# Performance work log

Measured on AMD Instinct MI355X. Metric: run time of the kernel, lower is better.

Reference implementation:

```python
import jax, jax.numpy as jnp
import numpy as np

B, Nv, Ne, Dv, De, Du = 8, 4096, 32768, 128, 128, 128
Dep, Dvp, Dup = 128, 128, 128


def setup_inputs() -> dict:
    key = jax.random.key(0)
    ks = jax.random.split(key, 11)
    s = 0.02
    return {
        "nodes": jax.random.normal(ks[0], (B, Nv, Dv), jnp.float32),
        "edges": jax.random.normal(ks[1], (B, Ne, De), jnp.float32),
        "global_u": jax.random.normal(ks[2], (B, Du), jnp.float32),
        "edge_rs": jax.random.randint(ks[3], (B, Ne, 2), 0, Nv, jnp.int32),
        "edge_masks": jax.random.randint(ks[4], (B, Ne, 1), 0, 2, jnp.int32),
        "W_edge": jax.random.normal(ks[5], (De + 2 * Dv + Du, Dep), jnp.float32) * s,
        "b_edge": jnp.zeros((Dep,), jnp.float32),
        "W_node": jax.random.normal(ks[6], (Dep + Dv + Du, Dvp), jnp.float32) * s,
        "b_node": jnp.zeros((Dvp,), jnp.float32),
        "W_glob": jax.random.normal(ks[7], (Dep + Dvp + Du, Dup), jnp.float32) * s,
        "b_glob": jnp.zeros((Dup,), jnp.float32),
    }


def reference(nodes, edges, global_u, edge_rs, edge_masks,
              W_edge, b_edge, W_node, b_node, W_glob, b_glob):
    recv = edge_rs[..., 0]  # (B,Ne)
    send = edge_rs[..., 1]
    # gather receiver / sender node features: (B,Ne,Dv)
    r_nodes = jnp.take_along_axis(nodes, jnp.broadcast_to(recv[..., None], (B, Ne, Dv)), axis=1)
    s_nodes = jnp.take_along_axis(nodes, jnp.broadcast_to(send[..., None], (B, Ne, Dv)), axis=1)
    u_e = jnp.broadcast_to(global_u[:, None, :], (B, Ne, Du))

    # edge block: MLP on concat -> (B,Ne,Dep)
    edge_in = jnp.concatenate([edges, r_nodes, s_nodes, u_e], -1)
    edges_p = jax.nn.relu(edge_in @ W_edge + b_edge)

    # e2v merge: masked segment-sum of edges onto receiver nodes -> (B,Nv,Dep)
    mask = edge_masks.astype(edges_p.dtype)  # (B,Ne,1)
    e2v = jax.vmap(lambda e, r: jax.ops.segment_sum(e, r, num_segments=Nv))(edges_p * mask, recv)

    # node block
    u_n = jnp.broadcast_to(global_u[:, None, :], (B, Nv, Du))
    node_in = jnp.concatenate([e2v, nodes, u_n], -1)
    nodes_p = jax.nn.relu(node_in @ W_node + b_node)

    # global block: sum-pool edges and nodes
    e2u = edges_p.sum(axis=1)  # (B,Dep)
    v2u = nodes_p.sum(axis=1)  # (B,Dvp)
    global_in = jnp.concatenate([e2u, v2u, global_u], -1)
    global_u_p = jax.nn.relu(global_in @ W_glob + b_glob)

    return (nodes_p, edges_p, global_u_p)
```

## Files before the change

### kernel.cpp

```cpp
#include <hip/hip_runtime.h>
#include <hip/hip_bf16.h>

#define B  8
#define NV 4096
#define NE 32768
#define D  128
#define KE2 384
#define KN2 256
#define KG 384

using short8 = __attribute__((ext_vector_type(8))) short;
using f32x4  = __attribute__((ext_vector_type(4))) float;

__device__ inline unsigned short f2bf(float f) {
    unsigned u = __builtin_bit_cast(unsigned, f);
    u += 0x7FFFu + ((u >> 16) & 1u);
    return (unsigned short)(u >> 16);
}

__device__ inline short8 cvt8(float4 a, float4 b) {
    union { __hip_bfloat162 h[4]; short8 v; } u;
    u.h[0] = __float22bfloat162_rn(make_float2(a.x, a.y));
    u.h[1] = __float22bfloat162_rn(make_float2(a.z, a.w));
    u.h[2] = __float22bfloat162_rn(make_float2(b.x, b.y));
    u.h[3] = __float22bfloat162_rn(make_float2(b.z, b.w));
    return u.v;
}

__global__ __launch_bounds__(256) void prep_weights(
    const float* __restrict__ We, const float* __restrict__ Wn,
    unsigned short* __restrict__ WtE, unsigned short* __restrict__ WtN)
{
    const int idx = blockIdx.x * 256 + threadIdx.x;
    {
        const int n = idx / KE2, k = idx % KE2;
        WtE[idx] = f2bf(We[(size_t)k * D + n]);
    }
    if (idx < 128 * KN2) {
        const int n = idx >> 8, k = idx & 255;
        WtN[idx] = f2bf(Wn[(size_t)k * D + n]);
    }
}

__global__ __launch_bounds__(128) void bias_kernel(
    const float* __restrict__ gu,
    const float* __restrict__ We, const float* __restrict__ be,
    const float* __restrict__ Wn, const float* __restrict__ bn,
    float* __restrict__ bias_e, float* __restrict__ bias_n)
{
    const int b = blockIdx.x, n = threadIdx.x;
    float se = be[n], sn = bn[n];
    for (int k = 0; k < D; ++k) {
        const float uk = gu[(size_t)b * D + k];
        se += uk * We[(size_t)(KE2 + k) * D + n];
        sn += uk * Wn[(size_t)(KN2 + k) * D + n];
    }
    bias_e[(size_t)b * D + n] = se;
    bias_n[(size_t)b * D + n] = sn;
}

__global__ __launch_bounds__(256) void hist_kernel(
    const int* __restrict__ edge_rs, const int* __restrict__ edge_masks,
    int* __restrict__ cnt)
{
    const int idx = blockIdx.x * 256 + threadIdx.x;
    if (edge_masks[idx]) {
        const int b = idx >> 15;
        const int r = edge_rs[2 * idx];
        atomicAdd(cnt + b * NV + r, 1);
    }
}

__global__ __launch_bounds__(1024) void scan_kernel(
    const int* __restrict__ cnt, int* __restrict__ off, int* __restrict__ cur)
{
    const int b = blockIdx.x, t = threadIdx.x;
    __shared__ int part[1024];
    int4 c = *(const int4*)(cnt + b * NV + t * 4);
    const int s0 = c.x, s1 = s0 + c.y, s2 = s1 + c.z, s3 = s2 + c.w;
    part[t] = s3;
    __syncthreads();
    #pragma unroll
    for (int d = 1; d < 1024; d <<= 1) {
        const int v = (t >= d) ? part[t - d] : 0;
        __syncthreads();
        part[t] += v;
        __syncthreads();
    }
    const int base = part[t] - s3;
    int* o = off + b * (NV + 1) + t * 4;
    o[0] = base; o[1] = base + s0; o[2] = base + s1; o[3] = base + s2;
    int4 cc = { base, base + s0, base + s1, base + s2 };
    *(int4*)(cur + b * NV + t * 4) = cc;
    if (t == 1023) off[b * (NV + 1) + NV] = part[1023];
}

__global__ __launch_bounds__(256) void scatter_kernel(
    const int* __restrict__ edge_rs, const int* __restrict__ edge_masks,
    int* __restrict__ cur, int* __restrict__ elist)
{
    const int idx = blockIdx.x * 256 + threadIdx.x;
    if (edge_masks[idx]) {
        const int b = idx >> 15;
        const int e = idx & (NE - 1);
        const int r = edge_rs[2 * idx];
        const int pos = atomicAdd(cur + b * NV + r, 1);
        elist[b * NE + pos] = e;
    }
}

__global__ __launch_bounds__(512, 4) void edge_kernel(
    const float* __restrict__ nodes,
    const float* __restrict__ edges,
    const int*   __restrict__ edge_rs,
    const unsigned short* __restrict__ WtE,
    const float* __restrict__ bias_e,
    float* __restrict__ edges_p,
    float* __restrict__ pe)
{
    __shared__ unsigned short Albuf[2][128 * 64];
    __shared__ unsigned short Wlbuf[2][128 * 64];

    const int tid  = threadIdx.x;
    const int bid  = blockIdx.x;
    const int b    = bid & 7;
    const int tile = bid >> 3;
    const int e0   = tile * 128;

    const int srow = tid >> 2;
    const int sq   = tid & 3;
    const int sX   = (srow & 7) << 3;

    const int2 rs = ((const int2*)edge_rs)[(size_t)b * NE + e0 + srow];
    const float* aseg0 = edges + ((size_t)b * NE + e0 + srow) * D;
    const float* aseg1 = nodes + ((size_t)b * NV + rs.x) * D;
    const float* aseg2 = nodes + ((size_t)b * NV + rs.y) * D;

    const int lane = tid & 63;
    const int wv   = tid >> 6;
    const int wr   = wv >> 2, wc = wv & 3;
    const int lc   = lane & 15, lg = lane >> 4;
    const int lX   = (lc & 7) << 3;

    float4 av[2], av2[2];
    short8 wstg[2];

    auto loadA = [&](int t) {
        const float* seg = (t < 2) ? aseg0 : (t < 4) ? aseg1 : aseg2;
        const float* src = seg + (t & 1) * 64 + sq * 16;
        av[0]  = *(const float4*)(src);
        av[1]  = *(const float4*)(src + 4);
        av2[0] = *(const float4*)(src + 8);
        av2[1] = *(const float4*)(src + 12);
    };
    auto loadW = [&](int t) {
        const unsigned short* src = WtE + (size_t)srow * KE2 + t * 64 + sq * 16;
        wstg[0] = *(const short8*)(src);
        wstg[1] = *(const short8*)(src + 8);
    };
    auto writeStage = [&](int buf) {
        unsigned short* Al = Albuf[buf];
        unsigned short* Wl = Wlbuf[buf];
        const int g0 = sq * 16;
        *(short8*)(Al + srow * 64 + ((g0    ) ^ sX)) = cvt8(av[0], av[1]);
        *(short8*)(Al + srow * 64 + ((g0 + 8) ^ sX)) = cvt8(av2[0], av2[1]);
        *(short8*)(Wl + srow * 64 + ((g0    ) ^ sX)) = wstg[0];
        *(short8*)(Wl + srow * 64 + ((g0 + 8) ^ sX)) = wstg[1];
    };

    f32x4 acc[4][2] = {};
    auto compute = [&](int buf) {
        const unsigned short* Al = Albuf[buf];
        const unsigned short* Wl = Wlbuf[buf];
        #pragma unroll
        for (int ksub = 0; ksub < 2; ++ksub) {
            const int k = ksub * 32 + lg * 8;
            short8 afr[4], bfr[2];
            #pragma unroll
            for (int mt = 0; mt < 4; ++mt)
                afr[mt] = *(const short8*)(Al + (wr * 64 + mt * 16 + lc) * 64 + (k ^ lX));
            #pragma unroll
            for (int nt = 0; nt < 2; ++nt)
                bfr[nt] = *(const short8*)(Wl + (wc * 32 + nt * 16 + lc) * 64 + (k ^ lX));
            #pragma unroll
            for (int mt = 0; mt < 4; ++mt)
                #pragma unroll
                for (int nt = 0; nt < 2; ++nt)
                    acc[mt][nt] = __builtin_amdgcn_mfma_f32_16x16x32_bf16(
                                      afr[mt], bfr[nt], acc[mt][nt], 0, 0, 0);
        }
    };

    loadA(0); loadW(0); writeStage(0);
    __syncthreads();
    #pragma unroll
    for (int t = 0; t < 6; ++t) {
        if (t < 5) { loadA(t + 1); loadW(t + 1); }
        compute(t & 1);
        if (t < 5) writeStage((t + 1) & 1);
        __syncthreads();
    }

    #pragma unroll
    for (int nt = 0; nt < 2; ++nt) {
        const int col = wc * 32 + nt * 16 + lc;
        const float bias = bias_e[(size_t)b * D + col];
        float csum = 0.f;
        #pragma unroll
        for (int mt = 0; mt < 4; ++mt)
            #pragma unroll
            for (int r = 0; r < 4; ++r) {
                const int row = wr * 64 + mt * 16 + lg * 4 + r;
                const float v = fmaxf(acc[mt][nt][r] + bias, 0.f);
                edges_p[((size_t)b * NE + e0 + row) * D + col] = v;
                csum += v;
            }
        csum += __shfl_xor(csum, 16);
        csum += __shfl_xor(csum, 32);
        if (lg == 0)
            pe[(((size_t)b * 256 + tile) * 2 + wr) * D + col] = csum;
    }
}

__global__ __launch_bounds__(512, 4) void node_kernel(
    const float* __restrict__ nodes,
    const float* __restrict__ edges_p,
    const int*   __restrict__ off,
    const int*   __restrict__ elist,
    const unsigned short* __restrict__ WtN,
    const float* __restrict__ bias_n,
    float* __restrict__ nodes_p,
    float* __restrict__ pn)
{
    __shared__ unsigned short Albuf[2][128 * 64];
    __shared__ unsigned short Wlbuf[2][128 * 64];

    const int tid  = threadIdx.x;
    const int bid  = blockIdx.x;
    const int b    = bid & 7;
    const int tile = bid >> 3;
    const int n0   = tile * 128;

    const int srow = tid >> 2;
    const int sq   = tid & 3;
    const int sX   = (srow & 7) << 3;

    const int vtx = n0 + srow;
    const int p0  = off[b * (NV + 1) + vtx];
    const int p1  = off[b * (NV + 1) + vtx + 1];
    const float* nsrc = nodes + ((size_t)b * NV + vtx) * D;

    const int lane = tid & 63;
    const int wv   = tid >> 6;
    const int wr   = wv >> 2, wc = wv & 3;
    const int lc   = lane & 15, lg = lane >> 4;
    const int lX   = (lc & 7) << 3;

    float4 av[2], av2[2];
    short8 wstg[2];

    auto loadA = [&](int t) {
        if (t < 2) {
            float4 s0 = {}, s1 = {}, s2 = {}, s3 = {};
            const int koff = (t & 1) * 64 + sq * 16;
            for (int p = p0; p < p1; ++p) {
                const int e = elist[b * NE + p];
                const float* src = edges_p + ((size_t)b * NE + e) * D + koff;
                const float4 x0 = *(const float4*)(src);
                const float4 x1 = *(const float4*)(src + 4);
                const float4 x2 = *(const float4*)(src + 8);
                const float4 x3 = *(const float4*)(src + 12);
                s0.x += x0.x; s0.y += x0.y; s0.z += x0.z; s0.w += x0.w;
                s1.x += x1.x; s1.y += x1.y; s1.z += x1.z; s1.w += x1.w;
                s2.x += x2.x; s2.y += x2.y; s2.z += x2.z; s2.w += x2.w;
                s3.x += x3.x; s3.y += x3.y; s3.z += x3.z; s3.w += x3.w;
            }
            av[0] = s0; av[1] = s1; av2[0] = s2; av2[1] = s3;
        } else {
            const float* src = nsrc + (t - 2) * 64 + sq * 16;
            av[0]  = *(const float4*)(src);
            av[1]  = *(const float4*)(src + 4);
            av2[0] = *(const float4*)(src + 8);
            av2[1] = *(const float4*)(src + 12);
        }
    };
    auto loadW = [&](int t) {
        const unsigned short* src = WtN + (size_t)srow * KN2 + t * 64 + sq * 16;
        wstg[0] = *(const short8*)(src);
        wstg[1] = *(const short8*)(src + 8);
    };
    auto writeStage = [&](int buf) {
        unsigned short* Al = Albuf[buf];
        unsigned short* Wl = Wlbuf[buf];
        const int g0 = sq * 16;
        *(short8*)(Al + srow * 64 + ((g0    ) ^ sX)) = cvt8(av[0], av[1]);
        *(short8*)(Al + srow * 64 + ((g0 + 8) ^ sX)) = cvt8(av2[0], av2[1]);
        *(short8*)(Wl + srow * 64 + ((g0    ) ^ sX)) = wstg[0];
        *(short8*)(Wl + srow * 64 + ((g0 + 8) ^ sX)) = wstg[1];
    };

    f32x4 acc[4][2] = {};
    auto compute = [&](int buf) {
        const unsigned short* Al = Albuf[buf];
        const unsigned short* Wl = Wlbuf[buf];
        #pragma unroll
        for (int ksub = 0; ksub < 2; ++ksub) {
            const int k = ksub * 32 + lg * 8;
            short8 afr[4], bfr[2];
            #pragma unroll
            for (int mt = 0; mt < 4; ++mt)
                afr[mt] = *(const short8*)(Al + (wr * 64 + mt * 16 + lc) * 64 + (k ^ lX));
            #pragma unroll
            for (int nt = 0; nt < 2; ++nt)
                bfr[nt] = *(const short8*)(Wl + (wc * 32 + nt * 16 + lc) * 64 + (k ^ lX));
            #pragma unroll
            for (int mt = 0; mt < 4; ++mt)
                #pragma unroll
                for (int nt = 0; nt < 2; ++nt)
                    acc[mt][nt] = __builtin_amdgcn_mfma_f32_16x16x32_bf16(
                                      afr[mt], bfr[nt], acc[mt][nt], 0, 0, 0);
        }
    };

    loadA(0); loadW(0); writeStage(0);
    __syncthreads();
    #pragma unroll
    for (int t = 0; t < 4; ++t) {
        if (t < 3) { loadA(t + 1); loadW(t + 1); }
        compute(t & 1);
        if (t < 3) writeStage((t + 1) & 1);
        __syncthreads();
    }

    #pragma unroll
    for (int nt = 0; nt < 2; ++nt) {
        const int col = wc * 32 + nt * 16 + lc;
        const float bias = bias_n[(size_t)b * D + col];
        float csum = 0.f;
        #pragma unroll
        for (int mt = 0; mt < 4; ++mt)
            #pragma unroll
            for (int r = 0; r < 4; ++r) {
                const int row = wr * 64 + mt * 16 + lg * 4 + r;
                const float v = fmaxf(acc[mt][nt][r] + bias, 0.f);
                nodes_p[((size_t)b * NV + n0 + row) * D + col] = v;
                csum += v;
            }
        csum += __shfl_xor(csum, 16);
        csum += __shfl_xor(csum, 32);
        if (lg == 0)
            pn[(((size_t)b * 32 + tile) * 2 + wr) * D + col] = csum;
    }
}

__global__ __launch_bounds__(128) void reduce_kernel(
    const float* __restrict__ pe, const float* __restrict__ pn,
    float* __restrict__ e2u, float* __restrict__ v2u)
{
    const int b = blockIdx.x, j = threadIdx.x;
    float s = 0.f;
    for (int i = 0; i < 512; ++i) s += pe[((size_t)b * 512 + i) * D + j];
    e2u[(size_t)b * D + j] = s;
    float t = 0.f;
    for (int i = 0; i < 64; ++i) t += pn[((size_t)b * 64 + i) * D + j];
    v2u[(size_t)b * D + j] = t;
}

__global__ __launch_bounds__(128) void glob_kernel(
    const float* __restrict__ e2u,
    const float* __restrict__ v2u,
    const float* __restrict__ gu,
    const float* __restrict__ W_glob,
    const float* __restrict__ b_glob,
    float* __restrict__ glob_p)
{
    __shared__ float gin[KG];
    const int b = blockIdx.x;
    const int j = threadIdx.x;

    gin[j      ] = e2u[(size_t)b * D + j];
    gin[j + 128] = v2u[(size_t)b * D + j];
    gin[j + 256] = gu [(size_t)b * D + j];
    __syncthreads();

    float acc = b_glob[j];
    #pragma unroll 4
    for (int k = 0; k < KG; ++k)
        acc += gin[k] * W_glob[(size_t)k * D + j];
    glob_p[(size_t)b * D + j] = fmaxf(acc, 0.f);
}

extern "C" void kernel_launch(void* const* d_in, const int* in_sizes, int n_in,
                              void* d_out, int out_size, void* d_ws, size_t ws_size,
                              hipStream_t stream) {
    const float* nodes      = (const float*)d_in[0];
    const float* edges      = (const float*)d_in[1];
    const float* gu         = (const float*)d_in[2];
    const int*   edge_rs    = (const int*)d_in[3];
    const int*   edge_masks = (const int*)d_in[4];
    const float* W_edge     = (const float*)d_in[5];
    const float* b_edge     = (const float*)d_in[6];
    const float* W_node     = (const float*)d_in[7];
    const float* b_node     = (const float*)d_in[8];
    const float* W_glob     = (const float*)d_in[9];
    const float* b_glob     = (const float*)d_in[10];

    float* out     = (float*)d_out;
    float* nodes_p = out;
    float* edges_p = out + (size_t)B * NV * D;
    float* glob_p  = edges_p + (size_t)B * NE * D;

    int*   cnt    = (int*)d_ws;
    int*   off    = cnt + (size_t)B * NV;
    int*   cur    = off + (size_t)B * (NV + 1);
    int*   elist  = cur + (size_t)B * NV;
    float* e2u    = (float*)(elist + (size_t)B * NE);
    float* v2u    = e2u + (size_t)B * D;
    float* bias_e = v2u + (size_t)B * D;
    float* bias_n = bias_e + (size_t)B * D;
    float* pe     = bias_n + (size_t)B * D;
    float* pn     = pe + (size_t)B * 512 * D;
    unsigned short* WtE = (unsigned short*)(pn + (size_t)B * 64 * D);
    unsigned short* WtN = WtE + 128 * KE2;

    hipMemsetAsync(cnt, 0, (size_t)B * NV * sizeof(int), stream);

    prep_weights<<<(128 * KE2) / 256, 256, 0, stream>>>(W_edge, W_node, WtE, WtN);
    bias_kernel<<<B, 128, 0, stream>>>(gu, W_edge, b_edge, W_node, b_node, bias_e, bias_n);
    hist_kernel<<<(B * NE) / 256, 256, 0, stream>>>(edge_rs, edge_masks, cnt);
    scan_kernel<<<B, 1024, 0, stream>>>(cnt, off, cur);
    scatter_kernel<<<(B * NE) / 256, 256, 0, stream>>>(edge_rs, edge_masks, cur, elist);

    edge_kernel<<<(NE / 128) * B, 512, 0, stream>>>(nodes, edges, edge_rs,
                                                    WtE, bias_e, edges_p, pe);
    node_kernel<<<(NV / 128) * B, 512, 0, stream>>>(nodes, edges_p, off, elist,
                                                    WtN, bias_n, nodes_p, pn);
    reduce_kernel<<<B, 128, 0, stream>>>(pe, pn, e2u, v2u);
    glob_kernel<<<B, 128, 0, stream>>>(e2u, v2u, gu, W_glob, b_glob, glob_p);
}
```

Measured before the change: 190.6 us.

## Keep full edge weight in LDS and give each wave its own edge rows

The edge kernel now loads the whole bf16 edge weight matrix into shared memory once per block. Each wave then processes 16 edges against all 128 output columns, staging its activations in a private double buffer, so the block-wide barriers inside the K loop are gone. Outputs are written as float4 and partial column sums are produced per wave, which grows the partial-sum buffer; the reduce kernel is widened to 256 threads to sum the larger buffer. The cost is much larger shared-memory use per block, which cuts resident blocks per CU and may limit latency hiding for the gather-heavy loads, plus a full weight reload from L2 into every block.

Result: slower. 226.1 us (+18.6%).

```diff
diff --git a/kernel.cpp b/kernel.cpp
--- a/kernel.cpp
+++ b/kernel.cpp
@@ -9,8 +9,9 @@
 #define KN2 256
 #define KG 384
 
-using short8 = __attribute__((ext_vector_type(8))) short;
-using f32x4  = __attribute__((ext_vector_type(4))) float;
+using short8    = __attribute__((ext_vector_type(8))) short;
+using f32x4     = __attribute__((ext_vector_type(4))) float;
+using ushort4_t = __attribute__((ext_vector_type(4))) unsigned short;
 
 __device__ inline unsigned short f2bf(float f) {
     unsigned u = __builtin_bit_cast(unsigned, f);
@@ -118,8 +119,8 @@
     float* __restrict__ edges_p,
     float* __restrict__ pe)
 {
-    __shared__ unsigned short Albuf[2][128 * 64];
-    __shared__ unsigned short Wlbuf[2][128 * 64];
+    __shared__ unsigned short Wsh[6 * 128 * 64];
+    __shared__ unsigned short Abuf[8 * 2 * 16 * 64];
 
     const int tid  = threadIdx.x;
     const int bid  = blockIdx.x;
@@ -127,98 +128,97 @@
     const int tile = bid >> 3;
     const int e0   = tile * 128;
 
-    const int srow = tid >> 2;
-    const int sq   = tid & 3;
-    const int sX   = (srow & 7) << 3;
-
-    const int2 rs = ((const int2*)edge_rs)[(size_t)b * NE + e0 + srow];
-    const float* aseg0 = edges + ((size_t)b * NE + e0 + srow) * D;
-    const float* aseg1 = nodes + ((size_t)b * NV + rs.x) * D;
-    const float* aseg2 = nodes + ((size_t)b * NV + rs.y) * D;
+    {
+        const int c  = tid >> 2;
+        const int q  = tid & 3;
+        const int sX = (c & 7) << 3;
+        #pragma unroll
+        for (int t = 0; t < 6; ++t) {
+            const unsigned short* src = WtE + (size_t)c * KE2 + t * 64 + q * 16;
+            unsigned short* dst = Wsh + t * 128 * 64 + c * 64;
+            *(short8*)(dst + ((q * 16    ) ^ sX)) = *(const short8*)(src);
+            *(short8*)(dst + ((q * 16 + 8) ^ sX)) = *(const short8*)(src + 8);
+        }
+    }
+    __syncthreads();
 
     const int lane = tid & 63;
     const int wv   = tid >> 6;
-    const int wr   = wv >> 2, wc = wv & 3;
-    const int lc   = lane & 15, lg = lane >> 4;
-    const int lX   = (lc & 7) << 3;
-
-    float4 av[2], av2[2];
-    short8 wstg[2];
-
+    const int lc   = lane & 15;
+    const int lg   = lane >> 4;
+    const int sXl  = (lc & 7) << 3;
+
+    const int    ew = e0 + wv * 16;
+    const size_t eb = (size_t)b * NE + ew + lc;
+    const int2   rs = ((const int2*)edge_rs)[eb];
+    const float* pE = edges + eb * D;
+    const float* pR = nodes + ((size_t)b * NV + rs.x) * D;
+    const float* pS = nodes + ((size_t)b * NV + rs.y) * D;
+
+    unsigned short* Aw = Abuf + wv * 2048;
+
+    float4 av[4];
     auto loadA = [&](int t) {
-        const float* seg = (t < 2) ? aseg0 : (t < 4) ? aseg1 : aseg2;
-        const float* src = seg + (t & 1) * 64 + sq * 16;
-        av[0]  = *(const float4*)(src);
-        av[1]  = *(const float4*)(src + 4);
-        av2[0] = *(const float4*)(src + 8);
-        av2[1] = *(const float4*)(src + 12);
-    };
-    auto loadW = [&](int t) {
-        const unsigned short* src = WtE + (size_t)srow * KE2 + t * 64 + sq * 16;
-        wstg[0] = *(const short8*)(src);
-        wstg[1] = *(const short8*)(src + 8);
-    };
-    auto writeStage = [&](int buf) {
-        unsigned short* Al = Albuf[buf];
-        unsigned short* Wl = Wlbuf[buf];
-        const int g0 = sq * 16;
-        *(short8*)(Al + srow * 64 + ((g0    ) ^ sX)) = cvt8(av[0], av[1]);
-        *(short8*)(Al + srow * 64 + ((g0 + 8) ^ sX)) = cvt8(av2[0], av2[1]);
-        *(short8*)(Wl + srow * 64 + ((g0    ) ^ sX)) = wstg[0];
-        *(short8*)(Wl + srow * 64 + ((g0 + 8) ^ sX)) = wstg[1];
-    };
-
-    f32x4 acc[4][2] = {};
-    auto compute = [&](int buf) {
-        const unsigned short* Al = Albuf[buf];
-        const unsigned short* Wl = Wlbuf[buf];
+        const float* seg = (t < 2) ? pE : (t < 4) ? pR : pS;
+        const float* src = seg + (t & 1) * 64 + lg * 16;
+        av[0] = *(const float4*)(src);
+        av[1] = *(const float4*)(src + 4);
+        av[2] = *(const float4*)(src + 8);
+        av[3] = *(const float4*)(src + 12);
+    };
+    auto writeA = [&](int buf) {
+        unsigned short* dst = Aw + buf * 1024 + lc * 64;
+        *(short8*)(dst + ((lg * 16    ) ^ sXl)) = cvt8(av[0], av[1]);
+        *(short8*)(dst + ((lg * 16 + 8) ^ sXl)) = cvt8(av[2], av[3]);
+    };
+
+    f32x4 acc[8] = {};
+    auto compute = [&](int t, int buf) {
+        const unsigned short* Asrc = Aw + buf * 1024;
+        const unsigned short* Wt   = Wsh + t * 128 * 64;
         #pragma unroll
         for (int ksub = 0; ksub < 2; ++ksub) {
             const int k = ksub * 32 + lg * 8;
-            short8 afr[4], bfr[2];
+            const short8 afr = *(const short8*)(Asrc + lc * 64 + (k ^ sXl));
             #pragma unroll
-            for (int mt = 0; mt < 4; ++mt)
-                afr[mt] = *(const short8*)(Al + (wr * 64 + mt * 16 + lc) * 64 + (k ^ lX));
-            #pragma unroll
-            for (int nt = 0; nt < 2; ++nt)
-                bfr[nt] = *(const short8*)(Wl + (wc * 32 + nt * 16 + lc) * 64 + (k ^ lX));
-            #pragma unroll
-            for (int mt = 0; mt < 4; ++mt)
-                #pragma unroll
-                for (int nt = 0; nt < 2; ++nt)
-                    acc[mt][nt] = __builtin_amdgcn_mfma_f32_16x16x32_bf16(
-                                      afr[mt], bfr[nt], acc[mt][nt], 0, 0, 0);
+            for (int nt = 0; nt < 8; ++nt) {
+                const int col = nt * 16 + lc;
+                const short8 bfr = *(const short8*)(Wt + col * 64 + (k ^ ((col & 7) << 3)));
+                acc[nt] = __builtin_amdgcn_mfma_f32_16x16x32_bf16(bfr, afr, acc[nt], 0, 0, 0);
+            }
         }
     };
 
-    loadA(0); loadW(0); writeStage(0);
-    __syncthreads();
+    loadA(0);
+    writeA(0);
     #pragma unroll
     for (int t = 0; t < 6; ++t) {
-        if (t < 5) { loadA(t + 1); loadW(t + 1); }
-        compute(t & 1);
-        if (t < 5) writeStage((t + 1) & 1);
-        __syncthreads();
+        if (t < 5) loadA(t + 1);
+        compute(t, t & 1);
+        if (t < 5) writeA((t + 1) & 1);
     }
 
     #pragma unroll
-    for (int nt = 0; nt < 2; ++nt) {
-        const int col = wc * 32 + nt * 16 + lc;
-        const float bias = bias_e[(size_t)b * D + col];
-        float csum = 0.f;
+    for (int nt = 0; nt < 8; ++nt) {
+        const int f0 = nt * 16 + lg * 4;
+        const float4 bb = *(const float4*)(bias_e + (size_t)b * D + f0);
+        float4 o;
+        o.x = fmaxf(acc[nt][0] + bb.x, 0.f);
+        o.y = fmaxf(acc[nt][1] + bb.y, 0.f);
+        o.z = fmaxf(acc[nt][2] + bb.z, 0.f);
+        o.w = fmaxf(acc[nt][3] + bb.w, 0.f);
+        *(float4*)(edges_p + eb * D + f0) = o;
+
+        float4 ps = o;
         #pragma unroll
-        for (int mt = 0; mt < 4; ++mt)
-            #pragma unroll
-            for (int r = 0; r < 4; ++r) {
-                const int row = wr * 64 + mt * 16 + lg * 4 + r;
-                const float v = fmaxf(acc[mt][nt][r] + bias, 0.f);
-                edges_p[((size_t)b * NE + e0 + row) * D + col] = v;
-                csum += v;
-            }
-        csum += __shfl_xor(csum, 16);
-        csum += __shfl_xor(csum, 32);
-        if (lg == 0)
-            pe[(((size_t)b * 256 + tile) * 2 + wr) * D + col] = csum;
+        for (int m = 1; m < 16; m <<= 1) {
+            ps.x += __shfl_xor(ps.x, m);
+            ps.y += __shfl_xor(ps.y, m);
+            ps.z += __shfl_xor(ps.z, m);
+            ps.w += __shfl_xor(ps.w, m);
+        }
+        if (lc == 0)
+            *(float4*)(pe + (((size_t)b * 256 + tile) * 8 + wv) * D + f0) = ps;
     }
 }
 
@@ -353,17 +353,27 @@
     }
 }
 
-__global__ __launch_bounds__(128) void reduce_kernel(
+__global__ __launch_bounds__(256) void reduce_kernel(
     const float* __restrict__ pe, const float* __restrict__ pn,
     float* __restrict__ e2u, float* __restrict__ v2u)
 {
-    const int b = blockIdx.x, j = threadIdx.x;
+    __shared__ float redE[2][128], redN[2][128];
+    const int b = blockIdx.x;
+    const int j = threadIdx.x & 127;
+    const int h = threadIdx.x >> 7;
     float s = 0.f;
-    for (int i = 0; i < 512; ++i) s += pe[((size_t)b * 512 + i) * D + j];
-    e2u[(size_t)b * D + j] = s;
+    for (int i = h * 1024; i < h * 1024 + 1024; ++i)
+        s += pe[((size_t)b * 2048 + i) * D + j];
     float t = 0.f;
-    for (int i = 0; i < 64; ++i) t += pn[((size_t)b * 64 + i) * D + j];
-    v2u[(size_t)b * D + j] = t;
+    for (int i = h * 32; i < h * 32 + 32; ++i)
+        t += pn[((size_t)b * 64 + i) * D + j];
+    redE[h][j] = s;
+    redN[h][j] = t;
+    __syncthreads();
+    if (h == 0) {
+        e2u[(size_t)b * D + j] = redE[0][j] + redE[1][j];
+        v2u[(size_t)b * D + j] = redN[0][j] + redN[1][j];
+    }
 }
 
 __global__ __launch_bounds__(128) void glob_kernel(
@@ -419,7 +429,7 @@
     float* bias_e = v2u + (size_t)B * D;
     float* bias_n = bias_e + (size_t)B * D;
     float* pe     = bias_n + (size_t)B * D;
-    float* pn     = pe + (size_t)B * 512 * D;
+    float* pn     = pe + (size_t)B * 2048 * D;
     unsigned short* WtE = (unsigned short*)(pn + (size_t)B * 64 * D);
     unsigned short* WtN = WtE + 128 * KE2;
 
@@ -435,6 +445,6 @@
                                                     WtE, bias_e, edges_p, pe);
     node_kernel<<<(NV / 128) * B, 512, 0, stream>>>(nodes, edges_p, off, elist,
                                                     WtN, bias_n, nodes_p, pn);
-    reduce_kernel<<<B, 128, 0, stream>>>(pe, pn, e2u, v2u);
+    reduce_kernel<<<B, 256, 0, stream>>>(pe, pn, e2u, v2u);
     glob_kernel<<<B, 128, 0, stream>>>(e2u, v2u, gu, W_glob, b_glob, glob_p);
 }
```
